# Performance work log

Measured on AMD Instinct MI355X. Metric: run time of the kernel, lower is better.

Reference implementation:

```python
import jax, jax.numpy as jnp
import numpy as np

SIZE = 7  # grid size; H = W = SIZE


def setup_inputs() -> dict:
    key = jax.random.key(0)
    k1, k2, k3, k4 = jax.random.split(key, 4)
    N, C = 256, 2048
    x = jax.random.normal(k1, (N, C, SIZE, SIZE), dtype=jnp.float32)
    mask = jax.random.uniform(k2, (N, SIZE, SIZE), dtype=jnp.float32)
    W = jax.random.normal(k3, (2, 2 * C), dtype=jnp.float32) * 0.02
    b = jax.random.normal(k4, (2,), dtype=jnp.float32) * 0.02
    return {"x": x, "mask": mask, "W": W, "b": b}


def reference(x, mask, W, b):
    N, C, H, Wd = x.shape
    HW = H * Wd
    size = float(H)
    # (N, HW, C) tokens
    reduced_x = jnp.transpose(x.reshape(N, C, HW), (0, 2, 1))
    m = mask.reshape(N, HW)
    thr = jnp.mean(m, axis=1, keepdims=True)  # curr_coef = 1.0
    binary_mask = (m > thr).astype(x.dtype)  # (N, HW)
    # mean over channels of masked tokens, then argmax over positions
    masked_mean = jnp.mean(reduced_x * binary_mask[:, :, None], axis=-1)  # (N, HW)
    max_index = jnp.argmax(masked_mean, axis=-1)  # (N,)
    batch_idx = jnp.arange(N)
    max_features = reduced_x[batch_idx, max_index]  # (N, C)
    # concat(max_feature, token) -> tiny linear 2C -> 2 with ReLU
    disc = jnp.concatenate(
        [jnp.broadcast_to(max_features[:, None, :], (N, HW, C)), reduced_x], axis=-1
    )  # (N, HW, 2C)
    preds_coord = jax.nn.relu(jnp.einsum('npc,oc->npo', disc, W) + b)  # (N, HW, 2)
    # zero out prediction at the anchor position
    preds_coord = preds_coord.at[batch_idx, max_index].set(0.0)
    # polar-coordinate targets relative to anchor
    ii, jj = jnp.meshgrid(jnp.arange(H), jnp.arange(Wd), indexing='ij')
    label = jnp.stack([ii, jj], axis=-1).astype(x.dtype).reshape(HW, 2)  # (HW, 2)
    basic_anchor = label[max_index][:, None, :]  # (N, 1, 2)
    rel = (label[None, :, :] - basic_anchor) / size  # (N, HW, 2)
    relative_dist = jnp.sqrt(jnp.sum(rel ** 2, axis=-1))  # (N, HW)
    relative_angle = jnp.arctan2(rel[:, :, 1], rel[:, :, 0])
    relative_angle = (relative_angle / jnp.float32(np.pi) + 1.0) / 2.0  # (N, HW)
    preds_dist = preds_coord[:, :, 0]
    preds_angle = preds_coord[:, :, 1]
    dist_loss = (preds_dist - relative_dist) ** 2
    gap = preds_angle - relative_angle
    gap = jnp.where(gap < 0, gap + 1.0, gap)
    gap = gap - jnp.mean(gap, axis=-1, keepdims=True)
    angle_loss = gap ** 2
    return (dist_loss + angle_loss).reshape(N, H, Wd)
```

## Files before the change

### kernel.cpp

```cpp
#include <hip/hip_runtime.h>
#include <math.h>

#define N_     256
#define C_     2048
#define HW_    49
#define CHUNKS 2
#define CPB    (C_/CHUNKS)
#define WCH    (CPB/4)
#define TILE_C 32
#define NTILE  (WCH/TILE_C)
#define NG     5
#define PARTS  (CHUNKS*4)
#define TBYTES (TILE_C*HW_*4)

__device__ __forceinline__ void cp16(const void* gptr, unsigned lds_off) {
  __builtin_amdgcn_global_load_lds(
      (const __attribute__((address_space(1))) unsigned int*)gptr,
      (__attribute__((address_space(3))) unsigned int*)lds_off,
      16, 0, 0);
}

__device__ __forceinline__ void stage_tile(const float* src, unsigned lb,
                                           int lane) {
  const char* s = (const char*)src;
  #pragma unroll
  for (int i = 0; i < 6; ++i)
    cp16(s + i*1024 + lane*16, lb + (unsigned)(i*1024));
  if (lane < 8)
    cp16(s + 6144 + lane*16, lb + 6144u);
}

__global__ __launch_bounds__(256) void k_reduce(const float* __restrict__ x,
                                                const float* __restrict__ Wm,
                                                float* __restrict__ part) {
  const int chunk = blockIdx.x;
  const int n     = blockIdx.y;
  const int t     = threadIdx.x;
  const int wave  = t >> 6;
  const int lane  = t & 63;

  __shared__ __align__(16) float buf[4][2][TILE_C*HW_];
  __shared__ float4 wt4[CPB];

  #pragma unroll
  for (int c = t; c < CPB; c += 256) {
    const int gc = chunk*CPB + c;
    float4 w;
    w.x = Wm[0*(2*C_)       + gc];
    w.y = Wm[1*(2*C_)       + gc];
    w.z = Wm[0*(2*C_) + C_  + gc];
    w.w = Wm[1*(2*C_) + C_  + gc];
    wt4[c] = w;
  }
  __syncthreads();

  const float* wbase = x + ((size_t)n*C_ + (size_t)chunk*CPB
                            + (size_t)wave*WCH)*HW_;
  const unsigned lb0 = (unsigned)(size_t)&buf[wave][0][0];
  const unsigned lb1 = (unsigned)(size_t)&buf[wave][1][0];

  stage_tile(wbase, lb0, lane);

  const int  p   = lane;
  const bool act = (lane < HW_);

  float a0 = 0.f, a1 = 0.f, a2 = 0.f, a3 = 0.f, a4 = 0.f;

  #pragma unroll 2
  for (int tt = 0; tt < NTILE; ++tt) {
    if (tt < NTILE-1) {
      stage_tile(wbase + (size_t)(tt+1)*TILE_C*HW_,
                 (tt & 1) ? lb0 : lb1, lane);
      asm volatile("s_waitcnt vmcnt(7)" ::: "memory");
    } else {
      asm volatile("s_waitcnt vmcnt(0)" ::: "memory");
    }

    if (act) {
      const float*  tl = &buf[wave][tt & 1][0];
      const float4* wp = &wt4[wave*WCH + tt*TILE_C];
      #pragma unroll 8
      for (int c = 0; c < TILE_C; ++c) {
        const float  v = tl[c*HW_ + p];
        const float4 w = wp[c];
        a0 += v;
        a1 = fmaf(v, w.x, a1);
        a2 = fmaf(v, w.y, a2);
        a3 = fmaf(v, w.z, a3);
        a4 = fmaf(v, w.w, a4);
      }
    }
    asm volatile("s_waitcnt lgkmcnt(0)" ::: "memory");
  }

  if (act) {
    float* dst = part + ((size_t)n*PARTS + (size_t)(chunk*4 + wave))*(NG*HW_);
    dst[0*HW_ + p] = a0;
    dst[1*HW_ + p] = a1;
    dst[2*HW_ + p] = a2;
    dst[3*HW_ + p] = a3;
    dst[4*HW_ + p] = a4;
  }
}

__global__ __launch_bounds__(256) void k_final(const float* __restrict__ part,
                                               const float* __restrict__ mask,
                                               const float* __restrict__ b,
                                               float* __restrict__ out) {
  const int n = blockIdx.x;
  const int t = threadIdx.x;
  __shared__ float red[NG*HW_];

  if (t < NG*HW_) {
    float a = 0.f;
    #pragma unroll
    for (int ch = 0; ch < PARTS; ++ch)
      a += part[((size_t)n*PARTS + ch)*(NG*HW_) + t];
    red[t] = a;
  }
  __syncthreads();

  if (t < 64) {
    const int  p   = t;
    const bool act = (p < HW_);

    float m = act ? mask[n*HW_ + p] : 0.f;
    float tot = m;
    #pragma unroll
    for (int off = 32; off; off >>= 1) tot += __shfl_xor(tot, off);
    const float thr = tot / 49.f;

    float s  = act ? red[0*HW_ + p] : 0.f;
    float mm = act ? ((m > thr) ? (s * (1.f/2048.f)) : 0.f) : -INFINITY;
    float best = mm;
    int   bidx = act ? p : 64;
    #pragma unroll
    for (int off = 32; off; off >>= 1) {
      float ov = __shfl_xor(best, off);
      int   oi = __shfl_xor(bidx, off);
      if (ov > best || (ov == best && oi < bidx)) { best = ov; bidx = oi; }
    }
    const int mi = bidx;

    const float u0mi = red[1*HW_ + mi];
    const float u1mi = red[2*HW_ + mi];

    float pred0 = 0.f, pred1 = 0.f;
    if (act) {
      pred0 = fmaxf(u0mi + red[3*HW_ + p] + b[0], 0.f);
      pred1 = fmaxf(u1mi + red[4*HW_ + p] + b[1], 0.f);
      if (p == mi) { pred0 = 0.f; pred1 = 0.f; }
    }

    const int ii = p / 7,  jj = p - ii*7;
    const int ai = mi / 7, aj = mi - ai*7;
    const float ri = (float)(ii - ai) / 7.f;
    const float rj = (float)(jj - aj) / 7.f;
    const float dist = sqrtf(ri*ri + rj*rj);
    const float ang  = (atan2f(rj, ri) / 3.14159274101257324f + 1.f) * 0.5f;

    float gap = pred1 - ang;
    if (gap < 0.f) gap += 1.f;
    float gsum = act ? gap : 0.f;
    #pragma unroll
    for (int off = 32; off; off >>= 1) gsum += __shfl_xor(gsum, off);
    const float gmean = gsum / 49.f;

    if (act) {
      const float dl = pred0 - dist;
      const float ga = gap - gmean;
      out[n*HW_ + p] = dl*dl + ga*ga;
    }
  }
}

extern "C" void kernel_launch(void* const* d_in, const int* in_sizes, int n_in,
                              void* d_out, int out_size, void* d_ws, size_t ws_size,
                              hipStream_t stream) {
  const float* x    = (const float*)d_in[0];
  const float* mask = (const float*)d_in[1];
  const float* Wm   = (const float*)d_in[2];
  const float* b    = (const float*)d_in[3];
  float* out  = (float*)d_out;
  float* part = (float*)d_ws;

  dim3 g1(CHUNKS, N_);
  k_reduce<<<g1, 256, 0, stream>>>(x, Wm, part);
  k_final<<<N_, 256, 0, stream>>>(part, mask, b, out);
}
```

Baseline: 159.0 us.

## Fuse reduce and finalize kernels into one 1024-thread block per sample

Merges the two kernels into one, so each block of 16 waves handles all channels of one sample. Per-wave partial sums are combined in LDS instead of through a global workspace, and the final loss is computed in the same block. This removes a kernel launch and the global round trip for partials. In exchange the grid shrinks to 256 large blocks with tiles half the old size, and LDS use grows to about 100 KB per block, which may lower occupancy and the amount of memory traffic in flight.

```diff
diff --git a/kernel.cpp b/kernel.cpp
--- a/kernel.cpp
+++ b/kernel.cpp
@@ -4,14 +4,12 @@
 #define N_     256
 #define C_     2048
 #define HW_    49
-#define CHUNKS 2
-#define CPB    (C_/CHUNKS)
-#define WCH    (CPB/4)
-#define TILE_C 32
+#define NW     16
+#define WCH    (C_/NW)
+#define TILE_C 16
 #define NTILE  (WCH/TILE_C)
 #define NG     5
-#define PARTS  (CHUNKS*4)
-#define TBYTES (TILE_C*HW_*4)
+#define TFLOAT (TILE_C*HW_)
 
 __device__ __forceinline__ void cp16(const void* gptr, unsigned lds_off) {
   __builtin_amdgcn_global_load_lds(
@@ -24,38 +22,39 @@
                                            int lane) {
   const char* s = (const char*)src;
   #pragma unroll
-  for (int i = 0; i < 6; ++i)
+  for (int i = 0; i < 3; ++i)
     cp16(s + i*1024 + lane*16, lb + (unsigned)(i*1024));
-  if (lane < 8)
-    cp16(s + 6144 + lane*16, lb + 6144u);
+  if (lane < 4)
+    cp16(s + 3072 + lane*16, lb + 3072u);
 }
 
-__global__ __launch_bounds__(256) void k_reduce(const float* __restrict__ x,
+__global__ __launch_bounds__(1024) void k_fused(const float* __restrict__ x,
+                                                const float* __restrict__ mask,
                                                 const float* __restrict__ Wm,
-                                                float* __restrict__ part) {
-  const int chunk = blockIdx.x;
-  const int n     = blockIdx.y;
-  const int t     = threadIdx.x;
-  const int wave  = t >> 6;
-  const int lane  = t & 63;
+                                                const float* __restrict__ b,
+                                                float* __restrict__ out) {
+  const int n    = blockIdx.x;
+  const int t    = threadIdx.x;
+  const int wave = t >> 6;
+  const int lane = t & 63;
 
-  __shared__ __align__(16) float buf[4][2][TILE_C*HW_];
-  __shared__ float4 wt4[CPB];
+  __shared__ __align__(16) float buf[NW][2][TFLOAT];
+  __shared__ float4 wt4[C_];
+  __shared__ float  red[NW][NG*HW_];
+  __shared__ float  rsum[NG*HW_];
 
   #pragma unroll
-  for (int c = t; c < CPB; c += 256) {
-    const int gc = chunk*CPB + c;
+  for (int c = t; c < C_; c += 1024) {
     float4 w;
-    w.x = Wm[0*(2*C_)       + gc];
-    w.y = Wm[1*(2*C_)       + gc];
-    w.z = Wm[0*(2*C_) + C_  + gc];
-    w.w = Wm[1*(2*C_) + C_  + gc];
+    w.x = Wm[c];
+    w.y = Wm[2*C_ + c];
+    w.z = Wm[C_   + c];
+    w.w = Wm[3*C_ + c];
     wt4[c] = w;
   }
   __syncthreads();
 
-  const float* wbase = x + ((size_t)n*C_ + (size_t)chunk*CPB
-                            + (size_t)wave*WCH)*HW_;
+  const float* wbase = x + ((size_t)n*C_ + (size_t)wave*WCH)*HW_;
   const unsigned lb0 = (unsigned)(size_t)&buf[wave][0][0];
   const unsigned lb1 = (unsigned)(size_t)&buf[wave][1][0];
 
@@ -69,9 +68,9 @@
   #pragma unroll 2
   for (int tt = 0; tt < NTILE; ++tt) {
     if (tt < NTILE-1) {
-      stage_tile(wbase + (size_t)(tt+1)*TILE_C*HW_,
+      stage_tile(wbase + (size_t)(tt+1)*TFLOAT,
                  (tt & 1) ? lb0 : lb1, lane);
-      asm volatile("s_waitcnt vmcnt(7)" ::: "memory");
+      asm volatile("s_waitcnt vmcnt(4)" ::: "memory");
     } else {
       asm volatile("s_waitcnt vmcnt(0)" ::: "memory");
     }
@@ -79,7 +78,7 @@
     if (act) {
       const float*  tl = &buf[wave][tt & 1][0];
       const float4* wp = &wt4[wave*WCH + tt*TILE_C];
-      #pragma unroll 8
+      #pragma unroll
       for (int c = 0; c < TILE_C; ++c) {
         const float  v = tl[c*HW_ + p];
         const float4 w = wp[c];
@@ -94,46 +93,36 @@
   }
 
   if (act) {
-    float* dst = part + ((size_t)n*PARTS + (size_t)(chunk*4 + wave))*(NG*HW_);
-    dst[0*HW_ + p] = a0;
-    dst[1*HW_ + p] = a1;
-    dst[2*HW_ + p] = a2;
-    dst[3*HW_ + p] = a3;
-    dst[4*HW_ + p] = a4;
+    red[wave][0*HW_ + p] = a0;
+    red[wave][1*HW_ + p] = a1;
+    red[wave][2*HW_ + p] = a2;
+    red[wave][3*HW_ + p] = a3;
+    red[wave][4*HW_ + p] = a4;
   }
-}
-
-__global__ __launch_bounds__(256) void k_final(const float* __restrict__ part,
-                                               const float* __restrict__ mask,
-                                               const float* __restrict__ b,
-                                               float* __restrict__ out) {
-  const int n = blockIdx.x;
-  const int t = threadIdx.x;
-  __shared__ float red[NG*HW_];
+  __syncthreads();
 
   if (t < NG*HW_) {
-    float a = 0.f;
+    float s = 0.f;
     #pragma unroll
-    for (int ch = 0; ch < PARTS; ++ch)
-      a += part[((size_t)n*PARTS + ch)*(NG*HW_) + t];
-    red[t] = a;
+    for (int w = 0; w < NW; ++w) s += red[w][t];
+    rsum[t] = s;
   }
   __syncthreads();
 
   if (t < 64) {
-    const int  p   = t;
-    const bool act = (p < HW_);
+    const int  pp  = t;
+    const bool ac  = (pp < HW_);
 
-    float m = act ? mask[n*HW_ + p] : 0.f;
+    float m = ac ? mask[n*HW_ + pp] : 0.f;
     float tot = m;
     #pragma unroll
     for (int off = 32; off; off >>= 1) tot += __shfl_xor(tot, off);
     const float thr = tot / 49.f;
 
-    float s  = act ? red[0*HW_ + p] : 0.f;
-    float mm = act ? ((m > thr) ? (s * (1.f/2048.f)) : 0.f) : -INFINITY;
+    float s  = ac ? rsum[0*HW_ + pp] : 0.f;
+    float mm = ac ? ((m > thr) ? (s * (1.f/2048.f)) : 0.f) : -INFINITY;
     float best = mm;
-    int   bidx = act ? p : 64;
+    int   bidx = ac ? pp : 64;
     #pragma unroll
     for (int off = 32; off; off >>= 1) {
       float ov = __shfl_xor(best, off);
@@ -142,18 +131,18 @@
     }
     const int mi = bidx;
 
-    const float u0mi = red[1*HW_ + mi];
-    const float u1mi = red[2*HW_ + mi];
+    const float u0mi = rsum[1*HW_ + mi];
+    const float u1mi = rsum[2*HW_ + mi];
 
     float pred0 = 0.f, pred1 = 0.f;
-    if (act) {
-      pred0 = fmaxf(u0mi + red[3*HW_ + p] + b[0], 0.f);
-      pred1 = fmaxf(u1mi + red[4*HW_ + p] + b[1], 0.f);
-      if (p == mi) { pred0 = 0.f; pred1 = 0.f; }
+    if (ac) {
+      pred0 = fmaxf(u0mi + rsum[3*HW_ + pp] + b[0], 0.f);
+      pred1 = fmaxf(u1mi + rsum[4*HW_ + pp] + b[1], 0.f);
+      if (pp == mi) { pred0 = 0.f; pred1 = 0.f; }
     }
 
-    const int ii = p / 7,  jj = p - ii*7;
-    const int ai = mi / 7, aj = mi - ai*7;
+    const int ii = pp / 7,  jj = pp - ii*7;
+    const int ai = mi / 7,  aj = mi - ai*7;
     const float ri = (float)(ii - ai) / 7.f;
     const float rj = (float)(jj - aj) / 7.f;
     const float dist = sqrtf(ri*ri + rj*rj);
@@ -161,15 +150,15 @@
 
     float gap = pred1 - ang;
     if (gap < 0.f) gap += 1.f;
-    float gsum = act ? gap : 0.f;
+    float gsum = ac ? gap : 0.f;
     #pragma unroll
     for (int off = 32; off; off >>= 1) gsum += __shfl_xor(gsum, off);
     const float gmean = gsum / 49.f;
 
-    if (act) {
+    if (ac) {
       const float dl = pred0 - dist;
       const float ga = gap - gmean;
-      out[n*HW_ + p] = dl*dl + ga*ga;
+      out[n*HW_ + pp] = dl*dl + ga*ga;
     }
   }
 }
@@ -182,9 +171,7 @@
   const float* Wm   = (const float*)d_in[2];
   const float* b    = (const float*)d_in[3];
   float* out  = (float*)d_out;
-  float* part = (float*)d_ws;
+  (void)d_ws; (void)ws_size;
 
-  dim3 g1(CHUNKS, N_);
-  k_reduce<<<g1, 256, 0, stream>>>(x, Wm, part);
-  k_final<<<N_, 256, 0, stream>>>(part, mask, b, out);
+  k_fused<<<dim3(N_), 1024, 0, stream>>>(x, mask, Wm, b, out);
 }
```

Measured after the change: 156.1 us. Within noise of the previous version (-1.8%).
